# Kernel tuning notes

Hardware: AMD Instinct MI355X
Metric: run time of the kernel (lower is better)

Reference implementation:

```python
import jax, jax.numpy as jnp
import numpy as np

D_MODEL = 2048
D_INNER = 2 * D_MODEL      # expand=2
D_STATE = 16
D_CONV = 4
DT_RANK = D_MODEL // 16    # ceil(2048/16)=128
BATCH, SEQLEN = 2, 1024


def setup_inputs() -> dict:
    key = jax.random.key(0)
    ks = jax.random.split(key, 10)
    s = 0.02
    inp = {
        "hidden_states": jax.random.normal(ks[0], (BATCH, SEQLEN, D_MODEL), jnp.float32),
        "in_proj_w": jax.random.normal(ks[1], (2 * D_INNER, D_MODEL), jnp.float32) * s,
        "conv_w": jax.random.normal(ks[2], (D_INNER, D_CONV), jnp.float32) * s,
        "conv_b": jax.random.normal(ks[3], (D_INNER,), jnp.float32) * s,
        "x_proj_w": jax.random.normal(ks[4], (DT_RANK + 2 * D_STATE, D_INNER), jnp.float32) * s,
        "dt_proj_w": jax.random.normal(ks[5], (D_INNER, DT_RANK), jnp.float32) * s,
        "dt_proj_b": jax.random.normal(ks[6], (D_INNER,), jnp.float32) * 0.1,
        "A_log": jnp.log(jnp.tile(jnp.arange(1, D_STATE + 1, dtype=jnp.float32), (D_INNER, 1))),
        "D": jnp.ones((D_INNER,), jnp.float32),
        "out_proj_w": jax.random.normal(ks[7], (D_MODEL, D_INNER), jnp.float32) * s,
    }
    return inp


def _mamba_forward(hidden_states, in_proj_w, conv_w, conv_b, x_proj_w,
                   dt_proj_w, dt_proj_b, A_log, D, out_proj_w):
    B, L, _ = hidden_states.shape
    # input projection -> x, z  (each [B, L, D_INNER])
    xz = jnp.einsum('bld,ed->ble', hidden_states, in_proj_w)
    x, z = jnp.split(xz, 2, axis=-1)
    # causal depthwise conv1d (kernel D_CONV) + SiLU
    x_pad = jnp.pad(x, ((0, 0), (D_CONV - 1, 0), (0, 0)))
    windows = jnp.stack([x_pad[:, k:k + L, :] for k in range(D_CONV)], axis=-1)  # [B,L,D,K]
    x_conv = jnp.einsum('bldk,dk->bld', windows, conv_w) + conv_b
    x_act = jax.nn.silu(x_conv)
    # data-dependent SSM parameters
    x_dbl = jnp.einsum('bld,ed->ble', x_act, x_proj_w)
    dt, Bc, Cc = jnp.split(x_dbl, [DT_RANK, DT_RANK + D_STATE], axis=-1)
    dt = jax.nn.softplus(jnp.einsum('blr,dr->bld', dt, dt_proj_w) + dt_proj_b)  # [B,L,D_INNER]
    A = -jnp.exp(A_log)  # [D_INNER, D_STATE]

    # selective scan over time (carry h: [B, D_INNER, D_STATE])
    def step(h, inp):
        x_t, dt_t, B_t, C_t = inp  # [B,D],[B,D],[B,N],[B,N]
        dA = jnp.exp(dt_t[:, :, None] * A[None])          # [B,D,N]
        dBx = dt_t[:, :, None] * B_t[:, None, :] * x_t[:, :, None]
        h = h * dA + dBx
        y = jnp.einsum('bdn,bn->bd', h, C_t)
        return h, y

    xs = (x_act.transpose(1, 0, 2), dt.transpose(1, 0, 2),
          Bc.transpose(1, 0, 2), Cc.transpose(1, 0, 2))
    h0 = jnp.zeros((B, D_INNER, D_STATE), x_act.dtype)
    _, ys = jax.lax.scan(step, h0, xs)          # [L,B,D_INNER]
    y = ys.transpose(1, 0, 2) + x_act * D       # skip connection D*x
    y = y * jax.nn.silu(z)                      # gating
    return jnp.einsum('bld,md->blm', y, out_proj_w)


def reference(hidden_states, in_proj_w, conv_w, conv_b, x_proj_w,
              dt_proj_w, dt_proj_b, A_log, D, out_proj_w):
    return _mamba_forward(hidden_states, in_proj_w, conv_w, conv_b, x_proj_w,
                          dt_proj_w, dt_proj_b, A_log, D, out_proj_w)
```

## Files before the change

kernel.cpp:

```cpp
#include <hip/hip_runtime.h>
#include <cstdint>
#include <cstddef>

#define D_MODEL 2048
#define D_INNER 4096
#define D_IN2   8192
#define D_STATE 16
#define D_CONVK 4
#define DT_RANK 128
#define BATCH   2
#define SEQLEN  1024
#define BL      (BATCH*SEQLEN)
#define XDBL_N  (DT_RANK + 2*D_STATE)
#define XPW_NPAD 256
#define XPROJ_SPLITS 8

#define NCHUNK  16
#define LCHUNK  (SEQLEN/NCHUNK)
#define CHW     (BATCH*D_INNER*D_STATE)

typedef short  s8v  __attribute__((ext_vector_type(8)));
typedef float  f4v  __attribute__((ext_vector_type(4)));

__device__ __forceinline__ float softplus_f(float v) {
    return (v > 20.f) ? v : log1pf(__expf(v));
}
__device__ __forceinline__ float silu_f(float v) {
    return v / (1.f + __expf(-v));
}
__device__ __forceinline__ float bf2f(short s) {
    return __uint_as_float(((uint32_t)(uint16_t)s) << 16);
}
__device__ __forceinline__ uint16_t f2bf(float f) {
    uint32_t u = __float_as_uint(f);
    return (uint16_t)((u + 0x7FFFu + ((u >> 16) & 1u)) >> 16);
}
__device__ __forceinline__ uint32_t packbf(float lo, float hi) {
    return ((uint32_t)f2bf(hi) << 16) | (uint32_t)f2bf(lo);
}
__device__ __forceinline__ float quad_sum(float p) {
    p += __int_as_float(__builtin_amdgcn_update_dpp(
            0, __float_as_int(p), 0xB1, 0xF, 0xF, true));
    p += __int_as_float(__builtin_amdgcn_update_dpp(
            0, __float_as_int(p), 0x4E, 0xF, 0xF, true));
    return p;
}

#define GLD16(gp, lp)                                                          \
    __builtin_amdgcn_global_load_lds(                                          \
        (const __attribute__((address_space(1))) void*)(gp),                   \
        (__attribute__((address_space(3))) void*)(lp), 16, 0, 0)

__global__ __launch_bounds__(256)
void cast_bf16_kernel(const float* __restrict__ in, uint32_t* __restrict__ out, int n8)
{
    const int i = blockIdx.x * 256 + threadIdx.x;
    if (i >= n8) return;
    const float4 a = ((const float4*)in)[i * 2];
    const float4 b = ((const float4*)in)[i * 2 + 1];
    uint4 o;
    o.x = packbf(a.x, a.y); o.y = packbf(a.z, a.w);
    o.z = packbf(b.x, b.y); o.w = packbf(b.z, b.w);
    ((uint4*)out)[i] = o;
}

template<int EPI>
__global__ __launch_bounds__(256)
void gemm_bf16_mfma(const short* __restrict__ A, int lda,
                    const short* __restrict__ W, int ldw,
                    const float* __restrict__ bias,
                    float* __restrict__ C, int ldc,
                    int M, int N, int K, int kchunk)
{
    __shared__ short sA[128 * 32];
    __shared__ short sW[128 * 32];

    const int tid = threadIdx.x;
    const int w   = tid >> 6;
    const int L   = tid & 63;
    const int bm  = blockIdx.y * 128;
    const int bn  = blockIdx.x * 128;
    const int k0  = blockIdx.z * kchunk;
    const int k1  = k0 + kchunk;
    C += (size_t)blockIdx.z * M * ldc;

    const int qa0 = 2 * w, qa1 = 2 * w + 1;
    const int srow = L >> 2;
    const int scol = (L & 3) * 8;

    const short* Ag0 = A + (size_t)(bm + qa0 * 16 + srow) * lda + scol;
    const short* Ag1 = A + (size_t)(bm + qa1 * 16 + srow) * lda + scol;
    const short* Wg0 = W + (size_t)(bn + qa0 * 16 + srow) * ldw + scol;
    const short* Wg1 = W + (size_t)(bn + qa1 * 16 + srow) * ldw + scol;

    const int wm = (w >> 1) * 64;
    const int wn = (w & 1) * 64;
    const int cl = L & 15;
    const int qd = L >> 4;

    f4v acc[4][4];
#pragma unroll
    for (int i = 0; i < 4; i++)
#pragma unroll
        for (int j = 0; j < 4; j++) acc[i][j] = (f4v){0.f, 0.f, 0.f, 0.f};

    for (int k = k0; k < k1; k += 32) {
        GLD16(Ag0 + k, &sA[qa0 * 512]);
        GLD16(Ag1 + k, &sA[qa1 * 512]);
        GLD16(Wg0 + k, &sW[qa0 * 512]);
        GLD16(Wg1 + k, &sW[qa1 * 512]);
        __syncthreads();

        s8v a[4], b[4];
#pragma unroll
        for (int mt = 0; mt < 4; mt++)
            a[mt] = *(const s8v*)&sA[(wm + mt * 16 + cl) * 32 + qd * 8];
#pragma unroll
        for (int nt = 0; nt < 4; nt++)
            b[nt] = *(const s8v*)&sW[(wn + nt * 16 + cl) * 32 + qd * 8];
#pragma unroll
        for (int mt = 0; mt < 4; mt++)
#pragma unroll
            for (int nt = 0; nt < 4; nt++)
                acc[mt][nt] = __builtin_amdgcn_mfma_f32_16x16x32_bf16(
                    a[mt], b[nt], acc[mt][nt], 0, 0, 0);
        __syncthreads();
    }

#pragma unroll
    for (int mt = 0; mt < 4; mt++) {
        const int row0 = bm + wm + mt * 16 + qd * 4;
#pragma unroll
        for (int nt = 0; nt < 4; nt++) {
            const int col = bn + wn + nt * 16 + cl;
#pragma unroll
            for (int r = 0; r < 4; r++) {
                float v = acc[mt][nt][r];
                if (EPI == 1) v = softplus_f(v + bias[col]);
                C[(size_t)(row0 + r) * ldc + col] = v;
            }
        }
    }
}

__global__ __launch_bounds__(256)
void conv_silu_kernel(const float* __restrict__ xz,
                      const float* __restrict__ cw,
                      const float* __restrict__ cb,
                      short* __restrict__ x_bf)
{
    const int idx = blockIdx.x * 256 + threadIdx.x;
    const int d  = idx & (D_INNER - 1);
    const int bl = idx >> 12;
    const int l  = bl & (SEQLEN - 1);
    const int b  = bl >> 10;
    const float* xb = xz + (size_t)b * SEQLEN * D_IN2 + d;
    float acc = cb[d];
#pragma unroll
    for (int k = 0; k < D_CONVK; k++) {
        const int ll = l + k - (D_CONVK - 1);
        if (ll >= 0) acc = fmaf(xb[(size_t)ll * D_IN2], cw[d * D_CONVK + k], acc);
    }
    x_bf[idx] = (short)f2bf(silu_f(acc));
}

__global__ __launch_bounds__(256)
void reduce_xdbl_kernel(const float* __restrict__ P,
                        float* __restrict__ xf,
                        short* __restrict__ xb)
{
    const int idx = blockIdx.x * 256 + threadIdx.x;
    if (idx >= BL * XDBL_N) return;
    const int m = idx / XDBL_N;
    const int n = idx - m * XDBL_N;
    float s = 0.f;
#pragma unroll
    for (int z = 0; z < XPROJ_SPLITS; z++)
        s += P[(size_t)z * BL * XPW_NPAD + (size_t)m * XPW_NPAD + n];
    xf[idx] = s;
    xb[idx] = (short)f2bf(s);
}


__global__ __launch_bounds__(256)
void scan_phase1(const short* __restrict__ x_bf, const float* __restrict__ dt,
                 const float* __restrict__ xdbl, const float* __restrict__ A_log,
                 float* __restrict__ h_end, float* __restrict__ Pprod)
{
    const int c   = blockIdx.y;
    const int ch0 = blockIdx.x * 64;
    const int b   = ch0 >> 12;
    const int d0  = ch0 & (D_INNER - 1);
    const int tid = threadIdx.x;
    const int g   = tid >> 2;
    const int q   = tid & 3;
    const int d   = d0 + g;

    const float4 Al = *(const float4*)&A_log[(d << 4) + (q << 2)];
    float An[4] = {-__expf(Al.x), -__expf(Al.y), -__expf(Al.z), -__expf(Al.w)};
    float h[4]  = {0.f, 0.f, 0.f, 0.f};
    float Pp[4] = {1.f, 1.f, 1.f, 1.f};

    __shared__ float s_x [16][68];
    __shared__ float s_dt[16][68];
    __shared__ float s_B [16][20];

    const int lt  = tid >> 4;
    const int ld4 = (tid & 15) * 4;

    for (int sub = 0; sub < LCHUNK / 16; sub++) {
        const int l0 = c * LCHUNK + sub * 16;
        const size_t bl = (size_t)(b * SEQLEN + l0 + lt);
        __syncthreads();
        {
            const short4 sx = *(const short4*)&x_bf[bl * D_INNER + d0 + ld4];
            const float4 dv = *(const float4*)&dt[bl * D_INNER + d0 + ld4];
            *(float4*)&s_x [lt][ld4] =
                make_float4(bf2f(sx.x), bf2f(sx.y), bf2f(sx.z), bf2f(sx.w));
            *(float4*)&s_dt[lt][ld4] = dv;
            if (tid < 64) {
                const int t2 = tid >> 2, k = (tid & 3) * 4;
                const size_t bl2 = (size_t)(b * SEQLEN + l0 + t2);
                *(float4*)&s_B[t2][k] =
                    *(const float4*)&xdbl[bl2 * XDBL_N + DT_RANK + k];
            }
        }
        __syncthreads();
#pragma unroll
        for (int t = 0; t < 16; t++) {
            const float xv  = s_x [t][g];
            const float dtv = s_dt[t][g];
            const float4 Bq = *(const float4*)&s_B[t][q * 4];
            const float Bv[4] = {Bq.x, Bq.y, Bq.z, Bq.w};
            const float dtx = dtv * xv;
#pragma unroll
            for (int j = 0; j < 4; j++) {
                const float dA = __expf(dtv * An[j]);
                h[j]  = fmaf(h[j], dA, dtx * Bv[j]);
                Pp[j] *= dA;
            }
        }
    }
    const size_t i0 = (size_t)c * CHW + (((size_t)(b * D_INNER + d)) << 4) + (q << 2);
    *(float4*)&h_end[i0] = make_float4(h[0], h[1], h[2], h[3]);
    *(float4*)&Pprod[i0] = make_float4(Pp[0], Pp[1], Pp[2], Pp[3]);
}

__global__ __launch_bounds__(256)
void scan_phase2(const float* __restrict__ h_end, const float* __restrict__ P,
                 float* __restrict__ h_in)
{
    const int i = blockIdx.x * 256 + threadIdx.x;
    float carry = 0.f;
#pragma unroll
    for (int c = 0; c < NCHUNK; c++) {
        h_in[(size_t)c * CHW + i] = carry;
        if (c < NCHUNK - 1)
            carry = fmaf(P[(size_t)c * CHW + i], carry, h_end[(size_t)c * CHW + i]);
    }
}

__global__ __launch_bounds__(256)
void scan_phase3(const short* __restrict__ x_bf, short* __restrict__ y_bf,
                 const float* __restrict__ dt, const float* __restrict__ xdbl,
                 const float* __restrict__ xz, const float* __restrict__ A_log,
                 const float* __restrict__ Dvec, const float* __restrict__ h_in)
{
    const int c   = blockIdx.y;
    const int ch0 = blockIdx.x * 64;
    const int b   = ch0 >> 12;
    const int d0  = ch0 & (D_INNER - 1);
    const int tid = threadIdx.x;
    const int g   = tid >> 2;
    const int q   = tid & 3;
    const int d   = d0 + g;

    const float4 Al = *(const float4*)&A_log[(d << 4) + (q << 2)];
    float An[4] = {-__expf(Al.x), -__expf(Al.y), -__expf(Al.z), -__expf(Al.w)};
    const float Dd = Dvec[d];
    const float4 h4 = *(const float4*)
        &h_in[(size_t)c * CHW + (((size_t)(b * D_INNER + d)) << 4) + (q << 2)];
    float h[4] = {h4.x, h4.y, h4.z, h4.w};

    __shared__ float s_x [16][68];
    __shared__ float s_dt[16][68];
    __shared__ float s_z [16][68];
    __shared__ float s_B [16][20];
    __shared__ float s_C [16][20];

    const int lt  = tid >> 4;
    const int ld4 = (tid & 15) * 4;

    for (int sub = 0; sub < LCHUNK / 16; sub++) {
        const int l0 = c * LCHUNK + sub * 16;
        const size_t bl = (size_t)(b * SEQLEN + l0 + lt);
        __syncthreads();
        {
            const short4 sx = *(const short4*)&x_bf[bl * D_INNER + d0 + ld4];
            const float4 dv = *(const float4*)&dt[bl * D_INNER + d0 + ld4];
            const float4 zv = *(const float4*)&xz[bl * D_IN2 + D_INNER + d0 + ld4];
            *(float4*)&s_x [lt][ld4] =
                make_float4(bf2f(sx.x), bf2f(sx.y), bf2f(sx.z), bf2f(sx.w));
            *(float4*)&s_dt[lt][ld4] = dv;
            *(float4*)&s_z [lt][ld4] = zv;
            if (tid < 128) {
                const int t2 = (tid & 63) >> 2, k = (tid & 3) * 4;
                const size_t bl2 = (size_t)(b * SEQLEN + l0 + t2);
                const int off = (tid < 64) ? 0 : D_STATE;
                const float4 v =
                    *(const float4*)&xdbl[bl2 * XDBL_N + DT_RANK + off + k];
                if (tid < 64) *(float4*)&s_B[t2][k] = v;
                else          *(float4*)&s_C[t2][k] = v;
            }
        }
        __syncthreads();
        const size_t orow = (size_t)(b * SEQLEN + l0);
#pragma unroll
        for (int t = 0; t < 16; t++) {
            const float xv  = s_x [t][g];
            const float dtv = s_dt[t][g];
            const float4 Bq = *(const float4*)&s_B[t][q * 4];
            const float4 Cq = *(const float4*)&s_C[t][q * 4];
            const float Bv[4] = {Bq.x, Bq.y, Bq.z, Bq.w};
            const float Cv[4] = {Cq.x, Cq.y, Cq.z, Cq.w};
            const float dtx = dtv * xv;
            float p = 0.f;
#pragma unroll
            for (int j = 0; j < 4; j++) {
                const float dA = __expf(dtv * An[j]);
                h[j] = fmaf(h[j], dA, dtx * Bv[j]);
                p = fmaf(h[j], Cv[j], p);
            }
            p = quad_sum(p);
            if (q == 0) {
                const float yv = fmaf(xv, Dd, p) * silu_f(s_z[t][g]);
                y_bf[(orow + t) * D_INNER + d] = (short)f2bf(yv);
            }
        }
    }
}

extern "C" void kernel_launch(void* const* d_in, const int* in_sizes, int n_in,
                              void* d_out, int out_size, void* d_ws, size_t ws_size,
                              hipStream_t stream)
{
    const float* hidden     = (const float*)d_in[0];
    const float* in_proj_w  = (const float*)d_in[1];
    const float* conv_w     = (const float*)d_in[2];
    const float* conv_b     = (const float*)d_in[3];
    const float* x_proj_w   = (const float*)d_in[4];
    const float* dt_proj_w  = (const float*)d_in[5];
    const float* dt_proj_b  = (const float*)d_in[6];
    const float* A_log      = (const float*)d_in[7];
    const float* Dvec       = (const float*)d_in[8];
    const float* out_proj_w = (const float*)d_in[9];
    float* out = (float*)d_out;

    const size_t MB = 1ull << 20;
    char* ws = (char*)d_ws;
    float* xz       = (float*)(ws);
    short* ipw_bf   = (short*)(ws + 64 * MB);
    short* x_bf     = (short*)(ws + 64 * MB);
    short* y_bf     = (short*)(ws + 80 * MB);
    float* h_end    = (float*)(ws + 80 * MB);
    float* Pbuf     = (float*)(ws + 88 * MB);
    float* dt_f32   = (float*)(ws + 96 * MB);
    float* P_part   = (float*)(ws + 96 * MB);
    short* opw_bf   = (short*)(ws + 96 * MB);
    float* h_in     = (float*)(ws + 128 * MB);
    short* hid_bf   = (short*)(ws + 128 * MB);
    short* xpw_bf   = (short*)(ws + 136 * MB);
    short* dtw_bf   = (short*)(ws + 138 * MB);
    float* xdbl_f   = (float*)(ws + 139 * MB);
    short* xdbl_bf  = (short*)(ws + 141 * MB);

    const dim3 blk(256);

    cast_bf16_kernel<<<dim3((BL * D_MODEL / 8 + 255) / 256), blk, 0, stream>>>(
        hidden, (uint32_t*)hid_bf, BL * D_MODEL / 8);
    cast_bf16_kernel<<<dim3((D_IN2 * D_MODEL / 8 + 255) / 256), blk, 0, stream>>>(
        in_proj_w, (uint32_t*)ipw_bf, D_IN2 * D_MODEL / 8);

    gemm_bf16_mfma<0><<<dim3(D_IN2 / 128, BL / 128, 1), blk, 0, stream>>>(
        hid_bf, D_MODEL, ipw_bf, D_MODEL, nullptr, xz, D_IN2, BL, D_IN2, D_MODEL, D_MODEL);

    conv_silu_kernel<<<dim3((BL * D_INNER) / 256), blk, 0, stream>>>(
        xz, conv_w, conv_b, x_bf);

    hipMemsetAsync(xpw_bf, 0, (size_t)XPW_NPAD * D_INNER * 2, stream);
    cast_bf16_kernel<<<dim3((XDBL_N * D_INNER / 8 + 255) / 256), blk, 0, stream>>>(
        x_proj_w, (uint32_t*)xpw_bf, XDBL_N * D_INNER / 8);
    gemm_bf16_mfma<0><<<dim3(XPW_NPAD / 128, BL / 128, XPROJ_SPLITS), blk, 0, stream>>>(
        x_bf, D_INNER, xpw_bf, D_INNER, nullptr, P_part, XPW_NPAD,
        BL, XPW_NPAD, D_INNER, D_INNER / XPROJ_SPLITS);
    reduce_xdbl_kernel<<<dim3((BL * XDBL_N + 255) / 256), blk, 0, stream>>>(
        P_part, xdbl_f, xdbl_bf);

    cast_bf16_kernel<<<dim3((D_INNER * DT_RANK / 8 + 255) / 256), blk, 0, stream>>>(
        dt_proj_w, (uint32_t*)dtw_bf, D_INNER * DT_RANK / 8);
    gemm_bf16_mfma<1><<<dim3(D_INNER / 128, BL / 128, 1), blk, 0, stream>>>(
        xdbl_bf, XDBL_N, dtw_bf, DT_RANK, dt_proj_b, dt_f32, D_INNER,
        BL, D_INNER, DT_RANK, DT_RANK);

    scan_phase1<<<dim3(BATCH * D_INNER / 64, NCHUNK - 1), blk, 0, stream>>>(
        x_bf, dt_f32, xdbl_f, A_log, h_end, Pbuf);
    scan_phase2<<<dim3(CHW / 256), blk, 0, stream>>>(h_end, Pbuf, h_in);
    scan_phase3<<<dim3(BATCH * D_INNER / 64, NCHUNK), blk, 0, stream>>>(
        x_bf, y_bf, dt_f32, xdbl_f, xz, A_log, Dvec, h_in);

    cast_bf16_kernel<<<dim3((D_MODEL * D_INNER / 8 + 255) / 256), blk, 0, stream>>>(
        out_proj_w, (uint32_t*)opw_bf, D_MODEL * D_INNER / 8);
    gemm_bf16_mfma<0><<<dim3(D_MODEL / 128, BL / 128, 1), blk, 0, stream>>>(
        y_bf, D_INNER, opw_bf, D_INNER, nullptr, out, D_MODEL,
        BL, D_MODEL, D_INNER, D_INNER);
}
```

Measured before the change: 537.9 us.

## Merge weight casts, store xz in bf16, widen GEMM K tile with swizzled LDS

Replaces the five separate fp32-to-bf16 cast launches with one multi-segment cast kernel. The in_proj GEMM now writes xz as bf16, which halves the write traffic and the later reads in conv and scan_phase3. The GEMM K step grows from 32 to 64 with an XOR-style rotated LDS layout, so there are half as many barriers per K and fewer LDS bank conflicts. The workspace layout is reshuffled to match, and the z gate and conv input lose precision from bf16 rounding.

```diff
diff --git a/kernel.cpp b/kernel.cpp
--- a/kernel.cpp
+++ b/kernel.cpp
@@ -19,6 +19,12 @@
 #define LCHUNK  (SEQLEN/NCHUNK)
 #define CHW     (BATCH*D_INNER*D_STATE)
 
+#define NB_HID  2048
+#define NB_IPW  8192
+#define NB_XPW  320
+#define NB_DTW  256
+#define NB_OPW  4096
+
 typedef short  s8v  __attribute__((ext_vector_type(8)));
 typedef float  f4v  __attribute__((ext_vector_type(4)));
 
@@ -52,16 +58,26 @@
         (__attribute__((address_space(3))) void*)(lp), 16, 0, 0)
 
 __global__ __launch_bounds__(256)
-void cast_bf16_kernel(const float* __restrict__ in, uint32_t* __restrict__ out, int n8)
-{
-    const int i = blockIdx.x * 256 + threadIdx.x;
-    if (i >= n8) return;
-    const float4 a = ((const float4*)in)[i * 2];
-    const float4 b = ((const float4*)in)[i * 2 + 1];
+void cast_all_kernel(const float* __restrict__ s0, uint32_t* __restrict__ d0,
+                     const float* __restrict__ s1, uint32_t* __restrict__ d1,
+                     const float* __restrict__ s2, uint32_t* __restrict__ d2,
+                     const float* __restrict__ s3, uint32_t* __restrict__ d3,
+                     const float* __restrict__ s4, uint32_t* __restrict__ d4)
+{
+    int blk = blockIdx.x;
+    const float* src; uint32_t* dst; int base;
+    if      (blk < NB_HID)                              { src = s0; dst = d0; base = blk; }
+    else if (blk < NB_HID + NB_IPW)                     { src = s1; dst = d1; base = blk - NB_HID; }
+    else if (blk < NB_HID + NB_IPW + NB_XPW)            { src = s2; dst = d2; base = blk - NB_HID - NB_IPW; }
+    else if (blk < NB_HID + NB_IPW + NB_XPW + NB_DTW)   { src = s3; dst = d3; base = blk - NB_HID - NB_IPW - NB_XPW; }
+    else                                                { src = s4; dst = d4; base = blk - NB_HID - NB_IPW - NB_XPW - NB_DTW; }
+    const int i = base * 256 + threadIdx.x;
+    const float4 a = ((const float4*)src)[i * 2];
+    const float4 b = ((const float4*)src)[i * 2 + 1];
     uint4 o;
     o.x = packbf(a.x, a.y); o.y = packbf(a.z, a.w);
     o.z = packbf(b.x, b.y); o.w = packbf(b.z, b.w);
-    ((uint4*)out)[i] = o;
+    ((uint4*)dst)[i] = o;
 }
 
 template<int EPI>
@@ -69,11 +85,11 @@
 void gemm_bf16_mfma(const short* __restrict__ A, int lda,
                     const short* __restrict__ W, int ldw,
                     const float* __restrict__ bias,
-                    float* __restrict__ C, int ldc,
+                    void* __restrict__ Cv, int ldc,
                     int M, int N, int K, int kchunk)
 {
-    __shared__ short sA[128 * 32];
-    __shared__ short sW[128 * 32];
+    __shared__ short sA[128 * 64];
+    __shared__ short sW[128 * 64];
 
     const int tid = threadIdx.x;
     const int w   = tid >> 6;
@@ -81,17 +97,15 @@
     const int bm  = blockIdx.y * 128;
     const int bn  = blockIdx.x * 128;
     const int k0  = blockIdx.z * kchunk;
-    const int k1  = k0 + kchunk;
-    C += (size_t)blockIdx.z * M * ldc;
-
-    const int qa0 = 2 * w, qa1 = 2 * w + 1;
-    const int srow = L >> 2;
-    const int scol = (L & 3) * 8;
-
-    const short* Ag0 = A + (size_t)(bm + qa0 * 16 + srow) * lda + scol;
-    const short* Ag1 = A + (size_t)(bm + qa1 * 16 + srow) * lda + scol;
-    const short* Wg0 = W + (size_t)(bn + qa0 * 16 + srow) * ldw + scol;
-    const short* Wg1 = W + (size_t)(bn + qa1 * 16 + srow) * ldw + scol;
+
+    const int rsub = L >> 3;
+    const int c8   = (((L & 7) - rsub) & 7) * 8;
+    const short* Ag[4]; const short* Wg[4];
+#pragma unroll
+    for (int j = 0; j < 4; j++) {
+        Ag[j] = A + (size_t)(bm + w * 32 + j * 8 + rsub) * lda + c8 + k0;
+        Wg[j] = W + (size_t)(bn + w * 32 + j * 8 + rsub) * ldw + c8 + k0;
+    }
 
     const int wm = (w >> 1) * 64;
     const int wn = (w & 1) * 64;
@@ -104,29 +118,36 @@
 #pragma unroll
         for (int j = 0; j < 4; j++) acc[i][j] = (f4v){0.f, 0.f, 0.f, 0.f};
 
-    for (int k = k0; k < k1; k += 32) {
-        GLD16(Ag0 + k, &sA[qa0 * 512]);
-        GLD16(Ag1 + k, &sA[qa1 * 512]);
-        GLD16(Wg0 + k, &sW[qa0 * 512]);
-        GLD16(Wg1 + k, &sW[qa1 * 512]);
-        __syncthreads();
-
-        s8v a[4], b[4];
-#pragma unroll
-        for (int mt = 0; mt < 4; mt++)
-            a[mt] = *(const s8v*)&sA[(wm + mt * 16 + cl) * 32 + qd * 8];
-#pragma unroll
-        for (int nt = 0; nt < 4; nt++)
-            b[nt] = *(const s8v*)&sW[(wn + nt * 16 + cl) * 32 + qd * 8];
-#pragma unroll
-        for (int mt = 0; mt < 4; mt++)
+    for (int k = 0; k < kchunk; k += 64) {
+#pragma unroll
+        for (int j = 0; j < 4; j++)
+            GLD16(Ag[j] + k, &sA[(w * 32 + j * 8) * 64]);
+#pragma unroll
+        for (int j = 0; j < 4; j++)
+            GLD16(Wg[j] + k, &sW[(w * 32 + j * 8) * 64]);
+        __syncthreads();
+#pragma unroll
+        for (int kk = 0; kk < 2; kk++) {
+            const int sl = ((kk * 4 + qd + cl) & 7) * 8;
+            s8v a[4], b[4];
+#pragma unroll
+            for (int mt = 0; mt < 4; mt++)
+                a[mt] = *(const s8v*)&sA[(wm + mt * 16 + cl) * 64 + sl];
 #pragma unroll
             for (int nt = 0; nt < 4; nt++)
-                acc[mt][nt] = __builtin_amdgcn_mfma_f32_16x16x32_bf16(
-                    a[mt], b[nt], acc[mt][nt], 0, 0, 0);
-        __syncthreads();
-    }
-
+                b[nt] = *(const s8v*)&sW[(wn + nt * 16 + cl) * 64 + sl];
+#pragma unroll
+            for (int mt = 0; mt < 4; mt++)
+#pragma unroll
+                for (int nt = 0; nt < 4; nt++)
+                    acc[mt][nt] = __builtin_amdgcn_mfma_f32_16x16x32_bf16(
+                        a[mt], b[nt], acc[mt][nt], 0, 0, 0);
+        }
+        __syncthreads();
+    }
+
+    float* Cf = (float*)Cv + (size_t)blockIdx.z * M * ldc;
+    short* Cs = (short*)Cv;
 #pragma unroll
     for (int mt = 0; mt < 4; mt++) {
         const int row0 = bm + wm + mt * 16 + qd * 4;
@@ -137,14 +158,15 @@
             for (int r = 0; r < 4; r++) {
                 float v = acc[mt][nt][r];
                 if (EPI == 1) v = softplus_f(v + bias[col]);
-                C[(size_t)(row0 + r) * ldc + col] = v;
-            }
-        }
-    }
-}
-
-__global__ __launch_bounds__(256)
-void conv_silu_kernel(const float* __restrict__ xz,
+                if (EPI == 2) Cs[(size_t)(row0 + r) * ldc + col] = (short)f2bf(v);
+                else          Cf[(size_t)(row0 + r) * ldc + col] = v;
+            }
+        }
+    }
+}
+
+__global__ __launch_bounds__(256)
+void conv_silu_kernel(const short* __restrict__ xz_bf,
                       const float* __restrict__ cw,
                       const float* __restrict__ cb,
                       short* __restrict__ x_bf)
@@ -154,12 +176,12 @@
     const int bl = idx >> 12;
     const int l  = bl & (SEQLEN - 1);
     const int b  = bl >> 10;
-    const float* xb = xz + (size_t)b * SEQLEN * D_IN2 + d;
+    const short* xb = xz_bf + (size_t)b * SEQLEN * D_IN2 + d;
     float acc = cb[d];
 #pragma unroll
     for (int k = 0; k < D_CONVK; k++) {
         const int ll = l + k - (D_CONVK - 1);
-        if (ll >= 0) acc = fmaf(xb[(size_t)ll * D_IN2], cw[d * D_CONVK + k], acc);
+        if (ll >= 0) acc = fmaf(bf2f(xb[(size_t)ll * D_IN2]), cw[d * D_CONVK + k], acc);
     }
     x_bf[idx] = (short)f2bf(silu_f(acc));
 }
@@ -180,7 +202,6 @@
     xf[idx] = s;
     xb[idx] = (short)f2bf(s);
 }
-
 
 __global__ __launch_bounds__(256)
 void scan_phase1(const short* __restrict__ x_bf, const float* __restrict__ dt,
@@ -263,7 +284,7 @@
 __global__ __launch_bounds__(256)
 void scan_phase3(const short* __restrict__ x_bf, short* __restrict__ y_bf,
                  const float* __restrict__ dt, const float* __restrict__ xdbl,
-                 const float* __restrict__ xz, const float* __restrict__ A_log,
+                 const short* __restrict__ xz_bf, const float* __restrict__ A_log,
                  const float* __restrict__ Dvec, const float* __restrict__ h_in)
 {
     const int c   = blockIdx.y;
@@ -298,11 +319,12 @@
         {
             const short4 sx = *(const short4*)&x_bf[bl * D_INNER + d0 + ld4];
             const float4 dv = *(const float4*)&dt[bl * D_INNER + d0 + ld4];
-            const float4 zv = *(const float4*)&xz[bl * D_IN2 + D_INNER + d0 + ld4];
+            const short4 zv = *(const short4*)&xz_bf[bl * D_IN2 + D_INNER + d0 + ld4];
             *(float4*)&s_x [lt][ld4] =
                 make_float4(bf2f(sx.x), bf2f(sx.y), bf2f(sx.z), bf2f(sx.w));
             *(float4*)&s_dt[lt][ld4] = dv;
-            *(float4*)&s_z [lt][ld4] = zv;
+            *(float4*)&s_z [lt][ld4] =
+                make_float4(bf2f(zv.x), bf2f(zv.y), bf2f(zv.z), bf2f(zv.w));
             if (tid < 128) {
                 const int t2 = (tid & 63) >> 2, k = (tid & 3) * 4;
                 const size_t bl2 = (size_t)(b * SEQLEN + l0 + t2);
@@ -358,46 +380,43 @@
 
     const size_t MB = 1ull << 20;
     char* ws = (char*)d_ws;
-    float* xz       = (float*)(ws);
-    short* ipw_bf   = (short*)(ws + 64 * MB);
-    short* x_bf     = (short*)(ws + 64 * MB);
-    short* y_bf     = (short*)(ws + 80 * MB);
-    float* h_end    = (float*)(ws + 80 * MB);
-    float* Pbuf     = (float*)(ws + 88 * MB);
-    float* dt_f32   = (float*)(ws + 96 * MB);
-    float* P_part   = (float*)(ws + 96 * MB);
-    short* opw_bf   = (short*)(ws + 96 * MB);
-    float* h_in     = (float*)(ws + 128 * MB);
-    short* hid_bf   = (short*)(ws + 128 * MB);
-    short* xpw_bf   = (short*)(ws + 136 * MB);
-    short* dtw_bf   = (short*)(ws + 138 * MB);
-    float* xdbl_f   = (float*)(ws + 139 * MB);
-    short* xdbl_bf  = (short*)(ws + 141 * MB);
+    short* xz_bf   = (short*)(ws);
+    short* x_bf    = (short*)(ws + 32 * MB);
+    short* ipw_bf  = (short*)(ws + 48 * MB);
+    short* y_bf    = (short*)(ws + 48 * MB);
+    float* h_end   = (float*)(ws + 64 * MB);
+    float* Pbuf    = (float*)(ws + 72 * MB);
+    short* hid_bf  = (short*)(ws + 80 * MB);
+    float* h_in    = (float*)(ws + 80 * MB);
+    short* opw_bf  = (short*)(ws + 88 * MB);
+    float* P_part  = (float*)(ws + 104 * MB);
+    float* dt_f32  = (float*)(ws + 104 * MB);
+    short* xpw_bf  = (short*)(ws + 136 * MB);
+    short* dtw_bf  = (short*)(ws + 138 * MB);
+    float* xdbl_f  = (float*)(ws + 139 * MB);
+    short* xdbl_bf = (short*)(ws + 139 * MB + 1310720);
 
     const dim3 blk(256);
 
-    cast_bf16_kernel<<<dim3((BL * D_MODEL / 8 + 255) / 256), blk, 0, stream>>>(
-        hidden, (uint32_t*)hid_bf, BL * D_MODEL / 8);
-    cast_bf16_kernel<<<dim3((D_IN2 * D_MODEL / 8 + 255) / 256), blk, 0, stream>>>(
-        in_proj_w, (uint32_t*)ipw_bf, D_IN2 * D_MODEL / 8);
-
-    gemm_bf16_mfma<0><<<dim3(D_IN2 / 128, BL / 128, 1), blk, 0, stream>>>(
-        hid_bf, D_MODEL, ipw_bf, D_MODEL, nullptr, xz, D_IN2, BL, D_IN2, D_MODEL, D_MODEL);
+    hipMemsetAsync(xpw_bf, 0, (size_t)XPW_NPAD * D_INNER * 2, stream);
+    cast_all_kernel<<<dim3(NB_HID + NB_IPW + NB_XPW + NB_DTW + NB_OPW), blk, 0, stream>>>(
+        hidden, (uint32_t*)hid_bf, in_proj_w, (uint32_t*)ipw_bf,
+        x_proj_w, (uint32_t*)xpw_bf, dt_proj_w, (uint32_t*)dtw_bf,
+        out_proj_w, (uint32_t*)opw_bf);
+
+    gemm_bf16_mfma<2><<<dim3(D_IN2 / 128, BL / 128, 1), blk, 0, stream>>>(
+        hid_bf, D_MODEL, ipw_bf, D_MODEL, nullptr, xz_bf, D_IN2,
+        BL, D_IN2, D_MODEL, D_MODEL);
 
     conv_silu_kernel<<<dim3((BL * D_INNER) / 256), blk, 0, stream>>>(
-        xz, conv_w, conv_b, x_bf);
-
-    hipMemsetAsync(xpw_bf, 0, (size_t)XPW_NPAD * D_INNER * 2, stream);
-    cast_bf16_kernel<<<dim3((XDBL_N * D_INNER / 8 + 255) / 256), blk, 0, stream>>>(
-        x_proj_w, (uint32_t*)xpw_bf, XDBL_N * D_INNER / 8);
+        xz_bf, conv_w, conv_b, x_bf);
+
     gemm_bf16_mfma<0><<<dim3(XPW_NPAD / 128, BL / 128, XPROJ_SPLITS), blk, 0, stream>>>(
         x_bf, D_INNER, xpw_bf, D_INNER, nullptr, P_part, XPW_NPAD,
         BL, XPW_NPAD, D_INNER, D_INNER / XPROJ_SPLITS);
     reduce_xdbl_kernel<<<dim3((BL * XDBL_N + 255) / 256), blk, 0, stream>>>(
         P_part, xdbl_f, xdbl_bf);
 
-    cast_bf16_kernel<<<dim3((D_INNER * DT_RANK / 8 + 255) / 256), blk, 0, stream>>>(
-        dt_proj_w, (uint32_t*)dtw_bf, D_INNER * DT_RANK / 8);
     gemm_bf16_mfma<1><<<dim3(D_INNER / 128, BL / 128, 1), blk, 0, stream>>>(
         xdbl_bf, XDBL_N, dtw_bf, DT_RANK, dt_proj_b, dt_f32, D_INNER,
         BL, D_INNER, DT_RANK, DT_RANK);
@@ -406,10 +425,8 @@
         x_bf, dt_f32, xdbl_f, A_log, h_end, Pbuf);
     scan_phase2<<<dim3(CHW / 256), blk, 0, stream>>>(h_end, Pbuf, h_in);
     scan_phase3<<<dim3(BATCH * D_INNER / 64, NCHUNK), blk, 0, stream>>>(
-        x_bf, y_bf, dt_f32, xdbl_f, xz, A_log, Dvec, h_in);
-
-    cast_bf16_kernel<<<dim3((D_MODEL * D_INNER / 8 + 255) / 256), blk, 0, stream>>>(
-        out_proj_w, (uint32_t*)opw_bf, D_MODEL * D_INNER / 8);
+        x_bf, y_bf, dt_f32, xdbl_f, xz_bf, A_log, Dvec, h_in);
+
     gemm_bf16_mfma<0><<<dim3(D_MODEL / 128, BL / 128, 1), blk, 0, stream>>>(
         y_bf, D_INNER, opw_bf, D_INNER, nullptr, out, D_MODEL,
         BL, D_MODEL, D_INNER, D_INNER);
```

After: 506.6 us. -5.8%, faster.
